# Performance work log

Measured on AMD Instinct MI355X. Metric: run time of the kernel, lower is better.

## Reference

```python
import jax, jax.numpy as jnp
import numpy as np

SCALE = 0.08838834764831845  # 1/sqrt(head_dim=128)
B, H, HKV, D = 32, 32, 8, 128
NUM_BLOCKS, BLOCK_SIZE, MAX_NUM_BLOCKS = 4096, 16, 256


def setup_inputs() -> dict:
    key = jax.random.key(0)
    ks = jax.random.split(key, 8)
    q = jax.random.normal(ks[0], (B, H, D), dtype=jnp.float32)
    k = jax.random.normal(ks[1], (B, HKV, D), dtype=jnp.float32)
    v = jax.random.normal(ks[2], (B, HKV, D), dtype=jnp.float32)
    k_cache = jax.random.normal(ks[3], (NUM_BLOCKS, BLOCK_SIZE, HKV, D), dtype=jnp.float32)
    v_cache = jax.random.normal(ks[4], (NUM_BLOCKS, BLOCK_SIZE, HKV, D), dtype=jnp.float32)
    slot_mapping = jax.random.randint(ks[5], (B,), 0, NUM_BLOCKS * BLOCK_SIZE, dtype=jnp.int32)
    block_tables = jax.random.randint(ks[6], (B, MAX_NUM_BLOCKS), 0, NUM_BLOCKS, dtype=jnp.int32)
    context_lens = jax.random.randint(ks[7], (B,), 0, MAX_NUM_BLOCKS * BLOCK_SIZE, dtype=jnp.int32)
    return {"q": q, "k": k, "v": v, "k_cache": k_cache, "v_cache": v_cache,
            "slot_mapping": slot_mapping, "block_tables": block_tables,
            "context_lens": context_lens}


def reference(q, k, v, k_cache, v_cache, slot_mapping, block_tables, context_lens):
    nb, bs, hkv, d = k_cache.shape
    b, h, _ = q.shape
    groups = h // hkv  # GQA repeat factor (repeat_interleave semantics)

    # --- store_kvcache: scatter the new decode token's k/v into the paged cache ---
    k_cache = k_cache.reshape(-1, hkv, d).at[slot_mapping].set(k).reshape(nb, bs, hkv, d)
    v_cache = v_cache.reshape(-1, hkv, d).at[slot_mapping].set(v).reshape(nb, bs, hkv, d)

    # --- block-table gather: [B, max_blocks] -> [B, T, HKV, D], T = max_blocks*bs ---
    t = block_tables.shape[1] * bs
    ids = jnp.maximum(block_tables, 0)  # clamp_min(0)
    k_tok = k_cache[ids].reshape(b, t, hkv, d)
    v_tok = v_cache[ids].reshape(b, t, hkv, d)

    # --- validity mask: block must be >=0 and token position < context_len ---
    pos = jnp.arange(t, dtype=jnp.int32)
    block_mask = jnp.repeat(block_tables >= 0, bs, axis=1)  # [B, T]
    valid = block_mask & (pos[None, :] < context_lens[:, None])
    has_tokens = valid.any(axis=1)  # [B]
    safe_valid = valid | ((~has_tokens)[:, None] & (pos[None, :] == 0))

    # --- attention (GQA via reshape instead of repeat_interleave materialization) ---
    qg = q.reshape(b, hkv, groups, d)  # head h = kv*groups + g matches repeat_interleave
    scores = jnp.einsum('bkgd,btkd->bkgt', qg, k_tok) * SCALE  # [B, HKV, G, T]
    scores = jnp.where(safe_valid[:, None, None, :], scores, -jnp.inf)
    w = jax.nn.softmax(scores.astype(jnp.float32), axis=-1).astype(q.dtype)
    o = jnp.einsum('bkgt,btkd->bkgd', w, v_tok).reshape(b, h, d)
    o = o * has_tokens[:, None, None].astype(o.dtype)
    return o[:, None, :, :]  # [B, 1, H, D] (matches transpose(1,2) of [B,H,1,D])
```

## Files before the change

### kernel.cpp

```cpp
#include <hip/hip_runtime.h>
#include <math.h>

#define B_ 32
#define H_ 32
#define HKV_ 8
#define G_ 4
#define D_ 128
#define BS_ 16
#define MAXNB_ 256
#define NSLOTS_ (4096 * 16)
#define SC_ (0.08838834764831845f * 1.4426950408889634f)
#define NEG_ -1e30f

__global__ void build_slot_map(const int* __restrict__ slot_mapping,
                               unsigned char* __restrict__ map) {
  const int tid = threadIdx.x;
  uint4* m4 = (uint4*)map;
#pragma unroll
  for (int i = 0; i < NSLOTS_ / 16 / 256; ++i)
    m4[tid + i * 256] = make_uint4(0u, 0u, 0u, 0u);
  __syncthreads();
  if (tid == 0) {
#pragma unroll
    for (int j = 0; j < B_; ++j)
      map[slot_mapping[j]] = (unsigned char)(j + 1);
  }
}

__global__ __launch_bounds__(256) void attn_split(
    const float* __restrict__ q,
    const float* __restrict__ k_new,
    const float* __restrict__ v_new,
    const float* __restrict__ k_cache,
    const float* __restrict__ v_cache,
    const int* __restrict__ block_tables,
    const int* __restrict__ context_lens,
    const unsigned char* __restrict__ map,
    float* __restrict__ O_part,
    float* __restrict__ M_part,
    float* __restrict__ L_part,
    int nsplit, int pps)
{
  __shared__ float Ml[4][4];
  __shared__ float Ll[4][4];
  __shared__ float Ob[4][4][128];

  const int tid = threadIdx.x;
  const int tok = tid >> 4;
  const int c = tid & 15;

  const int s  = blockIdx.x % nsplit;
  const int bk = blockIdx.x / nsplit;
  const int kv = bk % HKV_;
  const int b  = bk / HKV_;

  float qr[G_][8];
#pragma unroll
  for (int g = 0; g < G_; ++g) {
    const float* qp = q + ((size_t)(b * H_ + kv * G_ + g)) * D_ + c * 8;
    float4 a0 = *(const float4*)qp;
    float4 a1 = *(const float4*)(qp + 4);
    qr[g][0] = a0.x * SC_; qr[g][1] = a0.y * SC_;
    qr[g][2] = a0.z * SC_; qr[g][3] = a0.w * SC_;
    qr[g][4] = a1.x * SC_; qr[g][5] = a1.y * SC_;
    qr[g][6] = a1.z * SC_; qr[g][7] = a1.w * SC_;
  }

  float m2[G_], l[G_], o[G_][8];
#pragma unroll
  for (int g = 0; g < G_; ++g) {
    m2[g] = NEG_; l[g] = 0.f;
#pragma unroll
    for (int j = 0; j < 8; ++j) o[g][j] = 0.f;
  }

  const int ctx = context_lens[b];
  const int pages_total = (ctx + BS_ - 1) / BS_;
  const int p0 = s * pps;
  const int p1 = min(p0 + pps, pages_total);

  const int toff = tok * (HKV_ * D_) + kv * D_ + c * 8;

  float4 pk0, pk1, pv0, pv1;
  int pblk = 0;
  unsigned char pmap = 0;

  auto issue = [&](int pg) {
    pblk = block_tables[b * MAXNB_ + pg];
    int bc = pblk < 0 ? 0 : pblk;
    const float* kp = k_cache + (size_t)bc * (BS_ * HKV_ * D_) + toff;
    const float* vp = v_cache + (size_t)bc * (BS_ * HKV_ * D_) + toff;
    pmap = map[(size_t)bc * BS_ + tok];
    pk0 = *(const float4*)kp;
    pk1 = *(const float4*)(kp + 4);
    pv0 = *(const float4*)vp;
    pv1 = *(const float4*)(vp + 4);
  };

  if (p0 < p1) issue(p0);

  for (int pg = p0; pg < p1; ++pg) {
    float4 k0 = pk0, k1 = pk1, v0 = pv0, v1 = pv1;
    const int this_blk = pblk;
    const int m_cur = pmap;
    if (pg + 1 < p1) issue(pg + 1);

    if (m_cur != 0) {
      const int j = m_cur - 1;
      const float* kp = k_new + ((size_t)(j * HKV_ + kv)) * D_ + c * 8;
      const float* vp = v_new + ((size_t)(j * HKV_ + kv)) * D_ + c * 8;
      k0 = *(const float4*)kp; k1 = *(const float4*)(kp + 4);
      v0 = *(const float4*)vp; v1 = *(const float4*)(vp + 4);
    }

    float dt[G_];
#pragma unroll
    for (int g = 0; g < G_; ++g) {
      dt[g] = qr[g][0] * k0.x + qr[g][1] * k0.y + qr[g][2] * k0.z + qr[g][3] * k0.w
            + qr[g][4] * k1.x + qr[g][5] * k1.y + qr[g][6] * k1.z + qr[g][7] * k1.w;
    }
#pragma unroll
    for (int off = 1; off < 16; off <<= 1) {
#pragma unroll
      for (int g = 0; g < G_; ++g) dt[g] += __shfl_xor(dt[g], off, 16);
    }
    const int pos = pg * BS_ + tok;
    if ((pos < ctx) && (this_blk >= 0)) {
#pragma unroll
      for (int g = 0; g < G_; ++g) {
        float t2 = dt[g];
        float mn = fmaxf(m2[g], t2);
        float al = exp2f(m2[g] - mn);
        float p  = exp2f(t2 - mn);
        l[g] = l[g] * al + p;
        m2[g] = mn;
        o[g][0] = o[g][0] * al + p * v0.x;
        o[g][1] = o[g][1] * al + p * v0.y;
        o[g][2] = o[g][2] * al + p * v0.z;
        o[g][3] = o[g][3] * al + p * v0.w;
        o[g][4] = o[g][4] * al + p * v1.x;
        o[g][5] = o[g][5] * al + p * v1.y;
        o[g][6] = o[g][6] * al + p * v1.z;
        o[g][7] = o[g][7] * al + p * v1.w;
      }
    }
  }

#pragma unroll
  for (int off = 16; off < 64; off <<= 1) {
#pragma unroll
    for (int g = 0; g < G_; ++g) {
      float mo = __shfl_xor(m2[g], off, 64);
      float lo = __shfl_xor(l[g], off, 64);
      float mn = fmaxf(m2[g], mo);
      float f1 = exp2f(m2[g] - mn);
      float f2 = exp2f(mo - mn);
      l[g] = f1 * l[g] + f2 * lo;
      m2[g] = mn;
#pragma unroll
      for (int j = 0; j < 8; ++j)
        o[g][j] = f1 * o[g][j] + f2 * __shfl_xor(o[g][j], off, 64);
    }
  }

  const int w = tid >> 6;
  if ((tid & 63) == 0) {
#pragma unroll
    for (int g = 0; g < G_; ++g) { Ml[w][g] = m2[g]; Ll[w][g] = l[g]; }
  }
  if (((tid >> 4) & 3) == 0) {
#pragma unroll
    for (int g = 0; g < G_; ++g) {
      float* dst = &Ob[w][g][c * 8];
      *(float4*)dst       = make_float4(o[g][0], o[g][1], o[g][2], o[g][3]);
      *(float4*)(dst + 4) = make_float4(o[g][4], o[g][5], o[g][6], o[g][7]);
    }
  }
  __syncthreads();

  const int g2 = tid >> 6;
  const int dd = (tid & 63) * 2;
  float M = NEG_;
#pragma unroll
  for (int wv = 0; wv < 4; ++wv) M = fmaxf(M, Ml[wv][g2]);
  float Ls = 0.f, a0 = 0.f, a1 = 0.f;
#pragma unroll
  for (int wv = 0; wv < 4; ++wv) {
    float f = exp2f(Ml[wv][g2] - M);
    Ls += f * Ll[wv][g2];
    float2 ov = *(const float2*)&Ob[wv][g2][dd];
    a0 += f * ov.x;
    a1 += f * ov.y;
  }
  const size_t pi = ((size_t)((b * HKV_ + kv) * G_ + g2) * nsplit + s);
  O_part[pi * D_ + dd]     = a0;
  O_part[pi * D_ + dd + 1] = a1;
  if (dd == 0) { M_part[pi] = M; L_part[pi] = Ls; }
}

__global__ void combine_splits(const float* __restrict__ O_part,
                               const float* __restrict__ M_part,
                               const float* __restrict__ L_part,
                               const int* __restrict__ context_lens,
                               float* __restrict__ out, int nsplit) {
  const int blk = blockIdx.x;
  const int b = blk >> 5;
  const int d = threadIdx.x;
  const int ctx = context_lens[b];
  float r = 0.f;
  if (ctx > 0) {
    const size_t base = (size_t)blk * nsplit;
    float M = NEG_;
    for (int s = 0; s < nsplit; ++s) M = fmaxf(M, M_part[base + s]);
    float den = 0.f, acc = 0.f;
    for (int s = 0; s < nsplit; ++s) {
      float f = exp2f(M_part[base + s] - M);
      den += f * L_part[base + s];
      acc += f * O_part[(base + s) * D_ + d];
    }
    r = den > 0.f ? acc / den : 0.f;
  }
  out[(size_t)blk * D_ + d] = r;
}

extern "C" void kernel_launch(void* const* d_in, const int* in_sizes, int n_in,
                              void* d_out, int out_size, void* d_ws, size_t ws_size,
                              hipStream_t stream) {
  const float* q = (const float*)d_in[0];
  const float* k = (const float*)d_in[1];
  const float* v = (const float*)d_in[2];
  const float* k_cache = (const float*)d_in[3];
  const float* v_cache = (const float*)d_in[4];
  const int* slot_mapping = (const int*)d_in[5];
  const int* block_tables = (const int*)d_in[6];
  const int* context_lens = (const int*)d_in[7];
  float* out = (float*)d_out;

  const size_t map_bytes = NSLOTS_;
  unsigned char* map = (unsigned char*)d_ws;

  int nsplit = 16;
  while (nsplit > 1) {
    size_t need = map_bytes +
                  (size_t)B_ * HKV_ * G_ * nsplit * (D_ + 2) * sizeof(float);
    if (need <= ws_size) break;
    nsplit >>= 1;
  }
  float* O_part = (float*)((char*)d_ws + map_bytes);
  float* M_part = O_part + (size_t)B_ * HKV_ * G_ * nsplit * D_;
  float* L_part = M_part + (size_t)B_ * HKV_ * G_ * nsplit;
  int pps = MAXNB_ / nsplit;

  build_slot_map<<<1, 256, 0, stream>>>(slot_mapping, map);
  attn_split<<<B_ * HKV_ * nsplit, 256, 0, stream>>>(
      q, k, v, k_cache, v_cache, block_tables, context_lens, map,
      O_part, M_part, L_part, nsplit, pps);
  combine_splits<<<B_ * H_, D_, 0, stream>>>(O_part, M_part, L_part,
                                             context_lens, out, nsplit);
}
```

Measured before the change: 545.7 us.

## Balance split pages by context length and gate slot-map lookups with page mask

```diff
diff --git a/kernel.cpp b/kernel.cpp
--- a/kernel.cpp
+++ b/kernel.cpp
@@ -8,26 +8,35 @@
 #define D_ 128
 #define BS_ 16
 #define MAXNB_ 256
-#define NSLOTS_ (4096 * 16)
+#define NPAGES_ 4096
+#define NSLOTS_ (NPAGES_ * BS_)
 #define SC_ (0.08838834764831845f * 1.4426950408889634f)
 #define NEG_ -1e30f
 
 __global__ void build_slot_map(const int* __restrict__ slot_mapping,
-                               unsigned char* __restrict__ map) {
+                               unsigned char* __restrict__ map,
+                               unsigned int* __restrict__ pagemask) {
   const int tid = threadIdx.x;
   uint4* m4 = (uint4*)map;
 #pragma unroll
   for (int i = 0; i < NSLOTS_ / 16 / 256; ++i)
     m4[tid + i * 256] = make_uint4(0u, 0u, 0u, 0u);
+  uint4* p4 = (uint4*)pagemask;
+#pragma unroll
+  for (int i = 0; i < NPAGES_ * 4 / 16 / 256; ++i)
+    p4[tid + i * 256] = make_uint4(0u, 0u, 0u, 0u);
   __syncthreads();
   if (tid == 0) {
 #pragma unroll
-    for (int j = 0; j < B_; ++j)
-      map[slot_mapping[j]] = (unsigned char)(j + 1);
-  }
-}
-
-__global__ __launch_bounds__(256) void attn_split(
+    for (int j = 0; j < B_; ++j) {
+      int s = slot_mapping[j];
+      map[s] = (unsigned char)(j + 1);
+      pagemask[s >> 4] |= (1u << (s & 15));
+    }
+  }
+}
+
+__global__ __launch_bounds__(256, 2) void attn_split(
     const float* __restrict__ q,
     const float* __restrict__ k_new,
     const float* __restrict__ v_new,
@@ -36,10 +45,11 @@
     const int* __restrict__ block_tables,
     const int* __restrict__ context_lens,
     const unsigned char* __restrict__ map,
+    const unsigned int* __restrict__ pagemask,
     float* __restrict__ O_part,
     float* __restrict__ M_part,
     float* __restrict__ L_part,
-    int nsplit, int pps)
+    int nsplit)
 {
   __shared__ float Ml[4][4];
   __shared__ float Ll[4][4];
@@ -76,41 +86,55 @@
 
   const int ctx = context_lens[b];
   const int pages_total = (ctx + BS_ - 1) / BS_;
-  const int p0 = s * pps;
-  const int p1 = min(p0 + pps, pages_total);
+  const int p_per = (pages_total + nsplit - 1) / nsplit;
+  const int p0 = s * p_per;
+  const int p1 = min(p0 + p_per, pages_total);
 
   const int toff = tok * (HKV_ * D_) + kv * D_ + c * 8;
 
   float4 pk0, pk1, pv0, pv1;
   int pblk = 0;
-  unsigned char pmap = 0;
-
-  auto issue = [&](int pg) {
-    pblk = block_tables[b * MAXNB_ + pg];
+  unsigned int pmsk = 0;
+
+  if (p0 < p1) {
+    pblk = block_tables[b * MAXNB_ + p0];
     int bc = pblk < 0 ? 0 : pblk;
+    pmsk = pagemask[bc];
     const float* kp = k_cache + (size_t)bc * (BS_ * HKV_ * D_) + toff;
     const float* vp = v_cache + (size_t)bc * (BS_ * HKV_ * D_) + toff;
-    pmap = map[(size_t)bc * BS_ + tok];
     pk0 = *(const float4*)kp;
     pk1 = *(const float4*)(kp + 4);
     pv0 = *(const float4*)vp;
     pv1 = *(const float4*)(vp + 4);
-  };
-
-  if (p0 < p1) issue(p0);
+  }
 
   for (int pg = p0; pg < p1; ++pg) {
     float4 k0 = pk0, k1 = pk1, v0 = pv0, v1 = pv1;
     const int this_blk = pblk;
-    const int m_cur = pmap;
-    if (pg + 1 < p1) issue(pg + 1);
-
-    if (m_cur != 0) {
-      const int j = m_cur - 1;
-      const float* kp = k_new + ((size_t)(j * HKV_ + kv)) * D_ + c * 8;
-      const float* vp = v_new + ((size_t)(j * HKV_ + kv)) * D_ + c * 8;
-      k0 = *(const float4*)kp; k1 = *(const float4*)(kp + 4);
-      v0 = *(const float4*)vp; v1 = *(const float4*)(vp + 4);
+    const unsigned int this_msk = pmsk;
+
+    if (pg + 1 < p1) {
+      pblk = block_tables[b * MAXNB_ + pg + 1];
+      int bc = pblk < 0 ? 0 : pblk;
+      pmsk = pagemask[bc];
+      const float* kp = k_cache + (size_t)bc * (BS_ * HKV_ * D_) + toff;
+      const float* vp = v_cache + (size_t)bc * (BS_ * HKV_ * D_) + toff;
+      pk0 = *(const float4*)kp;
+      pk1 = *(const float4*)(kp + 4);
+      pv0 = *(const float4*)vp;
+      pv1 = *(const float4*)(vp + 4);
+    }
+
+    if (this_msk != 0) {
+      int bc = this_blk < 0 ? 0 : this_blk;
+      int mj = map[bc * BS_ + tok];
+      if (mj != 0) {
+        const int j = mj - 1;
+        const float* kp = k_new + ((size_t)(j * HKV_ + kv)) * D_ + c * 8;
+        const float* vp = v_new + ((size_t)(j * HKV_ + kv)) * D_ + c * 8;
+        k0 = *(const float4*)kp; k1 = *(const float4*)(kp + 4);
+        v0 = *(const float4*)vp; v1 = *(const float4*)(vp + 4);
+      }
     }
 
     float dt[G_];
@@ -237,24 +261,25 @@
   float* out = (float*)d_out;
 
   const size_t map_bytes = NSLOTS_;
+  const size_t pmask_bytes = NPAGES_ * sizeof(unsigned int);
   unsigned char* map = (unsigned char*)d_ws;
+  unsigned int* pagemask = (unsigned int*)((char*)d_ws + map_bytes);
 
   int nsplit = 16;
   while (nsplit > 1) {
-    size_t need = map_bytes +
+    size_t need = map_bytes + pmask_bytes +
                   (size_t)B_ * HKV_ * G_ * nsplit * (D_ + 2) * sizeof(float);
     if (need <= ws_size) break;
     nsplit >>= 1;
   }
-  float* O_part = (float*)((char*)d_ws + map_bytes);
+  float* O_part = (float*)((char*)d_ws + map_bytes + pmask_bytes);
   float* M_part = O_part + (size_t)B_ * HKV_ * G_ * nsplit * D_;
   float* L_part = M_part + (size_t)B_ * HKV_ * G_ * nsplit;
-  int pps = MAXNB_ / nsplit;
-
-  build_slot_map<<<1, 256, 0, stream>>>(slot_mapping, map);
+
+  build_slot_map<<<1, 256, 0, stream>>>(slot_mapping, map, pagemask);
   attn_split<<<B_ * HKV_ * nsplit, 256, 0, stream>>>(
-      q, k, v, k_cache, v_cache, block_tables, context_lens, map,
-      O_part, M_part, L_part, nsplit, pps);
+      q, k, v, k_cache, v_cache, block_tables, context_lens, map, pagemask,
+      O_part, M_part, L_part, nsplit);
   combine_splits<<<B_ * H_, D_, 0, stream>>>(O_part, M_part, L_part,
                                              context_lens, out, nsplit);
 }
```

New measurement: 515.6 us. 5.5% less time.
